# Kernel tuning notes

Hardware: AMD Instinct MI355X
Metric: run time of the kernel (lower is better)

## Reference

```python
import jax, jax.numpy as jnp
import numpy as np

DEPTH = 12
NODE_SIZE = 64
IN_SCALE = 1.0
SCALE = 0.1
IN_W = 1.8
SIZE = 2 ** DEPTH - 1          # 4095 total nodes
REST = SIZE - 1                # 4094 non-root nodes
M_BATCH = 128


def setup_inputs() -> dict:
    key = jax.random.key(0)
    k1, k2, k3 = jax.random.split(key, 3)
    weights = IN_W + 1e-4 * jax.random.normal(k1, (SIZE,), dtype=jnp.float32)
    noise_root = jax.random.normal(k2, (M_BATCH, NODE_SIZE, 1), dtype=jnp.float32)
    noise_rest = jax.random.normal(k3, (M_BATCH, NODE_SIZE, REST), dtype=jnp.float32)
    return {"weights": weights, "noise_root": noise_root, "noise_rest": noise_rest, "M": M_BATCH}


def reference(weights, noise_root, noise_rest, M):
    # Root: Normal(0, in_scale).rsample((M, node_size, 1))
    root = IN_SCALE * noise_root                      # (M, node, 1)
    samples_levels = [root]
    m_levels = []
    scale_levels = []
    off = 0
    for d in range(1, DEPTH):
        n = 2 ** d
        w = jax.nn.sigmoid(weights[off:off + n])       # (n,)
        parent = jnp.arange(n) // 2                    # half-index parent lookup
        m = w[None, None, :] * samples_levels[-1][:, :, parent]   # (M, node, n)
        sc = jnp.broadcast_to(((1.0 - w) * SCALE)[None, None, :], m.shape)
        samp = m + sc * noise_rest[:, :, off:off + n]  # reparameterized rsample
        samples_levels.append(samp)
        m_levels.append(m)
        scale_levels.append(sc)
        off += n
    samples = jnp.concatenate(samples_levels[::-1], axis=2)  # (M, node, 4095)
    ms = jnp.concatenate(m_levels[::-1], axis=2)              # (M, node, 4094)
    scales = jnp.concatenate(scale_levels[::-1], axis=2)      # (M, node, 4094)
    return samples, ms, scales
```

## Files before the change

kernel.cpp:

```cpp
#include <hip/hip_runtime.h>


constexpr int   kRows  = 8192;
constexpr float kScale = 0.1f;

typedef float f4_ __attribute__((ext_vector_type(4)));
typedef float f2_ __attribute__((ext_vector_type(2)));
typedef f4_ f4u __attribute__((aligned(4)));
typedef f2_ f2u __attribute__((aligned(4)));

__device__ __align__(16) float2 g_tab[4096];

__global__ __launch_bounds__(256) void lgt_precompute(
    const float* __restrict__ weights)
{
    int t = blockIdx.x * 256 + threadIdx.x;
    if (t < 4094) {
        int d = 31 - __clz(t + 2);
        int c = t + 4098 - 3 * (1 << d);
        float w = 1.0f / (1.0f + __expf(-weights[t]));
        g_tab[c] = make_float2(w, (1.0f - w) * kScale);
    }
}

__device__ __forceinline__ void lgkm_barrier() {
    __builtin_amdgcn_sched_barrier(0);
    asm volatile("s_waitcnt lgkmcnt(0)" ::: "memory");
    __builtin_amdgcn_s_barrier();
    __builtin_amdgcn_sched_barrier(0);
}

__global__ __launch_bounds__(256) void lgt_main(
    const float* __restrict__ noise_root,
    const float* __restrict__ noise_rest,
    float* __restrict__ samples,
    float* __restrict__ ms,
    float* __restrict__ scales)
{
    __shared__ float sL[256];

    const int row = blockIdx.x;
    const int tid = threadIdx.x;
    const float* __restrict__ nr = noise_rest + (size_t)row * 4094;
    float* __restrict__ sr = samples + (size_t)row * 4095;
    float* __restrict__ mr = ms      + (size_t)row * 4094;
    float* __restrict__ cr = scales  + (size_t)row * 4094;

    const float nzs = nr[tid];
    const float n8  = nr[254 + tid];
    const f2_  n9   = *(const f2_*)(nr + 510 + 2 * tid);
    const f2_  nA0  = *(const f2_*)(nr + 1022 + 4 * tid);
    const f2_  nA1  = *(const f2_*)(nr + 1022 + 4 * tid + 2);
    f2_ nL[4];
    #pragma unroll
    for (int k = 0; k < 4; ++k)
        nL[k] = *(const f2_*)(nr + 2046 + 8 * tid + 2 * k);
    const float rootv = noise_root[row];

    if (tid == 0) { sL[254] = rootv; sr[4094] = rootv; }
    lgkm_barrier();

    #pragma unroll
    for (int d = 1; d <= 7; ++d) {
        const int off     = (1 << d) - 2;
        const int n       = 1 << d;
        const int colbase = 4096 - (n << 1);
        if (tid >= off && tid < off + n) {
            const int c = colbase + (tid - off);
            const float2 t2 = g_tab[c];
            const float  p  = sL[(c >> 1) - 1792];
            const float  mv = t2.x * p;
            const float  v  = fmaf(t2.y, nzs, mv);
            sL[c - 3840] = v;
            sr[c] = v; mr[c] = mv; cr[c] = t2.y;
        }
        lgkm_barrier();
    }

    const float a7 = sL[tid >> 1];

    const float2 t8 = g_tab[3584 + tid];
    const float  m8 = t8.x * a7;
    const float  v8 = fmaf(t8.y, n8, m8);
    sr[3584 + tid] = v8; mr[3584 + tid] = m8; cr[3584 + tid] = t8.y;

    const f4_ t9 = *(const f4_*)(&g_tab[3072 + 2 * tid]);
    const float m90 = t9.x * v8, m91 = t9.z * v8;
    const float v90 = fmaf(t9.y, n9.x, m90);
    const float v91 = fmaf(t9.w, n9.y, m91);
    {
        f2_ sv; sv.x = v90; sv.y = v91;
        f2_ mv; mv.x = m90; mv.y = m91;
        f2_ cv; cv.x = t9.y; cv.y = t9.w;
        *(f2u*)(sr + 3072 + 2 * tid) = sv;
        *(f2_*)(mr + 3072 + 2 * tid) = mv;
        *(f2_*)(cr + 3072 + 2 * tid) = cv;
    }

    const f4_ tA = *(const f4_*)(&g_tab[2048 + 4 * tid]);
    const f4_ tB = *(const f4_*)(&g_tab[2048 + 4 * tid + 2]);
    const float mA0 = tA.x * v90, mA1 = tA.z * v90;
    const float mB0 = tB.x * v91, mB1 = tB.z * v91;
    const float vA0 = fmaf(tA.y, nA0.x, mA0);
    const float vA1 = fmaf(tA.w, nA0.y, mA1);
    const float vB0 = fmaf(tB.y, nA1.x, mB0);
    const float vB1 = fmaf(tB.w, nA1.y, mB1);
    {
        f4_ sv; sv.x = vA0; sv.y = vA1; sv.z = vB0; sv.w = vB1;
        f4_ mv; mv.x = mA0; mv.y = mA1; mv.z = mB0; mv.w = mB1;
        f4_ cv; cv.x = tA.y; cv.y = tA.w; cv.z = tB.y; cv.w = tB.w;
        *(f4u*)(sr + 2048 + 4 * tid) = sv;
        *(f4u*)(mr + 2048 + 4 * tid) = mv;
        *(f4u*)(cr + 2048 + 4 * tid) = cv;
    }

    const float pv0 = vA0, pv1 = vA1, pv2 = vB0, pv3 = vB1;
    float sv[8], mv[8], cv[8];
    #pragma unroll
    for (int k = 0; k < 4; ++k) {
        const f4_  t = *(const f4_*)(&g_tab[8 * tid + 2 * k]);
        const float p = (k == 0) ? pv0 : (k == 1) ? pv1 : (k == 2) ? pv2 : pv3;
        const float m0 = t.x * p, m1 = t.z * p;
        sv[2 * k]     = fmaf(t.y, nL[k].x, m0);
        sv[2 * k + 1] = fmaf(t.w, nL[k].y, m1);
        mv[2 * k] = m0; mv[2 * k + 1] = m1;
        cv[2 * k] = t.y; cv[2 * k + 1] = t.w;
    }
    {
        f4_ a, b;
        a.x = sv[0]; a.y = sv[1]; a.z = sv[2]; a.w = sv[3];
        b.x = sv[4]; b.y = sv[5]; b.z = sv[6]; b.w = sv[7];
        *(f4u*)(sr + 8 * tid)     = a;
        *(f4u*)(sr + 8 * tid + 4) = b;
        a.x = mv[0]; a.y = mv[1]; a.z = mv[2]; a.w = mv[3];
        b.x = mv[4]; b.y = mv[5]; b.z = mv[6]; b.w = mv[7];
        *(f4u*)(mr + 8 * tid)     = a;
        *(f4u*)(mr + 8 * tid + 4) = b;
        a.x = cv[0]; a.y = cv[1]; a.z = cv[2]; a.w = cv[3];
        b.x = cv[4]; b.y = cv[5]; b.z = cv[6]; b.w = cv[7];
        *(f4u*)(cr + 8 * tid)     = a;
        *(f4u*)(cr + 8 * tid + 4) = b;
    }
}

extern "C" void kernel_launch(void* const* d_in, const int* in_sizes, int n_in,
                              void* d_out, int out_size, void* d_ws, size_t ws_size,
                              hipStream_t stream)
{
    const float* weights    = (const float*)d_in[0];
    const float* noise_root = (const float*)d_in[1];
    const float* noise_rest = (const float*)d_in[2];

    float* out     = (float*)d_out;
    float* samples = out;
    float* ms      = samples + (size_t)kRows * 4095;
    float* scales  = ms      + (size_t)kRows * 4094;

    lgt_precompute<<<(4094 + 255) / 256, 256, 0, stream>>>(weights);
    lgt_main<<<kRows, 256, 0, stream>>>(noise_root, noise_rest,
                                        samples, ms, scales);
}
```

Before: 120.3 us.

## Split tree sampling into wave-per-row top kernel and barrier-free bulk kernel

Drops the sigmoid precompute table and computes sigmoid weights inline from the weights array. The shallow levels (1-7) are now done by a separate kernel, one wavefront per row, using shuffles instead of shared memory and block barriers. The bulk kernel then reads the level-7 values back from the samples output in global memory. This removes the serial barrier chain in each block of the main kernel. In exchange it adds a global round-trip for the level-7 values, a kernel launch, and extra transcendental work in every block.

Measured after the change: 130.5 us. +8.5%, slower.

```diff
diff --git a/kernel.cpp b/kernel.cpp
--- a/kernel.cpp
+++ b/kernel.cpp
@@ -9,137 +9,164 @@
 typedef f4_ f4u __attribute__((aligned(4)));
 typedef f2_ f2u __attribute__((aligned(4)));
 
-__device__ __align__(16) float2 g_tab[4096];
-
-__global__ __launch_bounds__(256) void lgt_precompute(
-    const float* __restrict__ weights)
-{
-    int t = blockIdx.x * 256 + threadIdx.x;
-    if (t < 4094) {
-        int d = 31 - __clz(t + 2);
-        int c = t + 4098 - 3 * (1 << d);
-        float w = 1.0f / (1.0f + __expf(-weights[t]));
-        g_tab[c] = make_float2(w, (1.0f - w) * kScale);
-    }
+__device__ __forceinline__ float sigm(float x) {
+    return 1.0f / (1.0f + __expf(-x));
 }
 
-__device__ __forceinline__ void lgkm_barrier() {
-    __builtin_amdgcn_sched_barrier(0);
-    asm volatile("s_waitcnt lgkmcnt(0)" ::: "memory");
-    __builtin_amdgcn_s_barrier();
-    __builtin_amdgcn_sched_barrier(0);
-}
-
-__global__ __launch_bounds__(256) void lgt_main(
+__global__ __launch_bounds__(256) void lgt_top(
+    const float* __restrict__ weights,
     const float* __restrict__ noise_root,
     const float* __restrict__ noise_rest,
     float* __restrict__ samples,
     float* __restrict__ ms,
     float* __restrict__ scales)
 {
-    __shared__ float sL[256];
-
-    const int row = blockIdx.x;
-    const int tid = threadIdx.x;
+    const int lane = threadIdx.x & 63;
+    const int row  = (blockIdx.x << 2) + (threadIdx.x >> 6);
     const float* __restrict__ nr = noise_rest + (size_t)row * 4094;
     float* __restrict__ sr = samples + (size_t)row * 4095;
     float* __restrict__ mr = ms      + (size_t)row * 4094;
     float* __restrict__ cr = scales  + (size_t)row * 4094;
 
-    const float nzs = nr[tid];
-    const float n8  = nr[254 + tid];
-    const f2_  n9   = *(const f2_*)(nr + 510 + 2 * tid);
-    const f2_  nA0  = *(const f2_*)(nr + 1022 + 4 * tid);
-    const f2_  nA1  = *(const f2_*)(nr + 1022 + 4 * tid + 2);
-    f2_ nL[4];
+    const float rootv = noise_root[row];
+    if (lane == 0) sr[4094] = rootv;
+
+    float v = rootv;
     #pragma unroll
-    for (int k = 0; k < 4; ++k)
-        nL[k] = *(const f2_*)(nr + 2046 + 8 * tid + 2 * k);
-    const float rootv = noise_root[row];
-
-    if (tid == 0) { sL[254] = rootv; sr[4094] = rootv; }
-    lgkm_barrier();
-
-    #pragma unroll
-    for (int d = 1; d <= 7; ++d) {
+    for (int d = 1; d <= 6; ++d) {
         const int off     = (1 << d) - 2;
         const int n       = 1 << d;
         const int colbase = 4096 - (n << 1);
-        if (tid >= off && tid < off + n) {
-            const int c = colbase + (tid - off);
-            const float2 t2 = g_tab[c];
-            const float  p  = sL[(c >> 1) - 1792];
-            const float  mv = t2.x * p;
-            const float  v  = fmaf(t2.y, nzs, mv);
-            sL[c - 3840] = v;
-            sr[c] = v; mr[c] = mv; cr[c] = t2.y;
+        const float p  = (d == 1) ? rootv : __shfl(v, lane >> 1);
+        const float wt = weights[off + lane];
+        const float nz = nr[off + lane];
+        const float w  = sigm(wt);
+        const float sc = (1.0f - w) * kScale;
+        const float m  = w * p;
+        v = fmaf(sc, nz, m);
+        if (lane < n) {
+            const int c = colbase + lane;
+            sr[c] = v; mr[c] = m; cr[c] = sc;
         }
-        lgkm_barrier();
     }
 
-    const float a7 = sL[tid >> 1];
+    {
+        const f2_ wt = *(const f2_*)(weights + 126 + 2 * lane);
+        const f2_ nz = *(const f2_*)(nr + 126 + 2 * lane);
+        const float w0  = sigm(wt.x), w1 = sigm(wt.y);
+        const float sc0 = (1.0f - w0) * kScale, sc1 = (1.0f - w1) * kScale;
+        const float m0  = w0 * v, m1 = w1 * v;
+        const float v0  = fmaf(sc0, nz.x, m0), v1 = fmaf(sc1, nz.y, m1);
+        const int   c   = 3840 + 2 * lane;
+        f2_ sv; sv.x = v0;  sv.y = v1;
+        f2_ mv; mv.x = m0;  mv.y = m1;
+        f2_ cv; cv.x = sc0; cv.y = sc1;
+        *(f2u*)(sr + c) = sv;
+        *(f2_*)(mr + c) = mv;
+        *(f2_*)(cr + c) = cv;
+    }
+}
 
-    const float2 t8 = g_tab[3584 + tid];
-    const float  m8 = t8.x * a7;
-    const float  v8 = fmaf(t8.y, n8, m8);
-    sr[3584 + tid] = v8; mr[3584 + tid] = m8; cr[3584 + tid] = t8.y;
+__global__ __launch_bounds__(256) void lgt_bulk(
+    const float* __restrict__ weights,
+    const float* __restrict__ noise_rest,
+    float*  samples,
+    float* __restrict__ ms,
+    float* __restrict__ scales)
+{
+    const int row = blockIdx.x;
+    const int s   = threadIdx.x;
+    const float* __restrict__ nr = noise_rest + (size_t)row * 4094;
+    float* sr = samples + (size_t)row * 4095;
+    float* __restrict__ mr = ms     + (size_t)row * 4094;
+    float* __restrict__ cr = scales + (size_t)row * 4094;
 
-    const f4_ t9 = *(const f4_*)(&g_tab[3072 + 2 * tid]);
-    const float m90 = t9.x * v8, m91 = t9.z * v8;
-    const float v90 = fmaf(t9.y, n9.x, m90);
-    const float v91 = fmaf(t9.w, n9.y, m91);
+    const float a7 = sr[3840 + (s >> 1)];
+
+    const float w8t = weights[254 + s];
+    const f2_  w9t  = *(const f2_*)(weights + 510  + 2 * s);
+    const f2_  wA0  = *(const f2_*)(weights + 1022 + 4 * s);
+    const f2_  wA1  = *(const f2_*)(weights + 1022 + 4 * s + 2);
+    f2_ wB[4];
+    #pragma unroll
+    for (int k = 0; k < 4; ++k)
+        wB[k] = *(const f2_*)(weights + 2046 + 8 * s + 2 * k);
+
+    const float n8 = nr[254 + s];
+    const f2_  n9  = *(const f2_*)(nr + 510  + 2 * s);
+    const f2_  nA0 = *(const f2_*)(nr + 1022 + 4 * s);
+    const f2_  nA1 = *(const f2_*)(nr + 1022 + 4 * s + 2);
+    f2_ nB[4];
+    #pragma unroll
+    for (int k = 0; k < 4; ++k)
+        nB[k] = *(const f2_*)(nr + 2046 + 8 * s + 2 * k);
+
+    const float w8  = sigm(w8t);
+    const float c8  = (1.0f - w8) * kScale;
+    const float m8  = w8 * a7;
+    const float v8  = fmaf(c8, n8, m8);
+    sr[3584 + s] = v8; mr[3584 + s] = m8; cr[3584 + s] = c8;
+
+    const float w90 = sigm(w9t.x), w91 = sigm(w9t.y);
+    const float c90 = (1.0f - w90) * kScale, c91 = (1.0f - w91) * kScale;
+    const float m90 = w90 * v8, m91 = w91 * v8;
+    const float v90 = fmaf(c90, n9.x, m90);
+    const float v91 = fmaf(c91, n9.y, m91);
     {
         f2_ sv; sv.x = v90; sv.y = v91;
         f2_ mv; mv.x = m90; mv.y = m91;
-        f2_ cv; cv.x = t9.y; cv.y = t9.w;
-        *(f2u*)(sr + 3072 + 2 * tid) = sv;
-        *(f2_*)(mr + 3072 + 2 * tid) = mv;
-        *(f2_*)(cr + 3072 + 2 * tid) = cv;
+        f2_ cv; cv.x = c90; cv.y = c91;
+        *(f2u*)(sr + 3072 + 2 * s) = sv;
+        *(f2_*)(mr + 3072 + 2 * s) = mv;
+        *(f2_*)(cr + 3072 + 2 * s) = cv;
     }
 
-    const f4_ tA = *(const f4_*)(&g_tab[2048 + 4 * tid]);
-    const f4_ tB = *(const f4_*)(&g_tab[2048 + 4 * tid + 2]);
-    const float mA0 = tA.x * v90, mA1 = tA.z * v90;
-    const float mB0 = tB.x * v91, mB1 = tB.z * v91;
-    const float vA0 = fmaf(tA.y, nA0.x, mA0);
-    const float vA1 = fmaf(tA.w, nA0.y, mA1);
-    const float vB0 = fmaf(tB.y, nA1.x, mB0);
-    const float vB1 = fmaf(tB.w, nA1.y, mB1);
+    const float wa0 = sigm(wA0.x), wa1 = sigm(wA0.y);
+    const float wa2 = sigm(wA1.x), wa3 = sigm(wA1.y);
+    const float ca0 = (1.0f - wa0) * kScale, ca1 = (1.0f - wa1) * kScale;
+    const float ca2 = (1.0f - wa2) * kScale, ca3 = (1.0f - wa3) * kScale;
+    const float mA0 = wa0 * v90, mA1 = wa1 * v90;
+    const float mA2 = wa2 * v91, mA3 = wa3 * v91;
+    const float vA0 = fmaf(ca0, nA0.x, mA0);
+    const float vA1 = fmaf(ca1, nA0.y, mA1);
+    const float vA2 = fmaf(ca2, nA1.x, mA2);
+    const float vA3 = fmaf(ca3, nA1.y, mA3);
     {
-        f4_ sv; sv.x = vA0; sv.y = vA1; sv.z = vB0; sv.w = vB1;
-        f4_ mv; mv.x = mA0; mv.y = mA1; mv.z = mB0; mv.w = mB1;
-        f4_ cv; cv.x = tA.y; cv.y = tA.w; cv.z = tB.y; cv.w = tB.w;
-        *(f4u*)(sr + 2048 + 4 * tid) = sv;
-        *(f4u*)(mr + 2048 + 4 * tid) = mv;
-        *(f4u*)(cr + 2048 + 4 * tid) = cv;
+        f4_ sv; sv.x = vA0; sv.y = vA1; sv.z = vA2; sv.w = vA3;
+        f4_ mv; mv.x = mA0; mv.y = mA1; mv.z = mA2; mv.w = mA3;
+        f4_ cv; cv.x = ca0; cv.y = ca1; cv.z = ca2; cv.w = ca3;
+        *(f4u*)(sr + 2048 + 4 * s) = sv;
+        *(f4u*)(mr + 2048 + 4 * s) = mv;
+        *(f4u*)(cr + 2048 + 4 * s) = cv;
     }
 
-    const float pv0 = vA0, pv1 = vA1, pv2 = vB0, pv3 = vB1;
+    const float pv[4] = { vA0, vA1, vA2, vA3 };
     float sv[8], mv[8], cv[8];
     #pragma unroll
     for (int k = 0; k < 4; ++k) {
-        const f4_  t = *(const f4_*)(&g_tab[8 * tid + 2 * k]);
-        const float p = (k == 0) ? pv0 : (k == 1) ? pv1 : (k == 2) ? pv2 : pv3;
-        const float m0 = t.x * p, m1 = t.z * p;
-        sv[2 * k]     = fmaf(t.y, nL[k].x, m0);
-        sv[2 * k + 1] = fmaf(t.w, nL[k].y, m1);
-        mv[2 * k] = m0; mv[2 * k + 1] = m1;
-        cv[2 * k] = t.y; cv[2 * k + 1] = t.w;
+        const float wb0 = sigm(wB[k].x), wb1 = sigm(wB[k].y);
+        const float cb0 = (1.0f - wb0) * kScale, cb1 = (1.0f - wb1) * kScale;
+        const float p   = pv[k];
+        const float mb0 = wb0 * p, mb1 = wb1 * p;
+        sv[2 * k]     = fmaf(cb0, nB[k].x, mb0);
+        sv[2 * k + 1] = fmaf(cb1, nB[k].y, mb1);
+        mv[2 * k] = mb0; mv[2 * k + 1] = mb1;
+        cv[2 * k] = cb0; cv[2 * k + 1] = cb1;
     }
     {
         f4_ a, b;
         a.x = sv[0]; a.y = sv[1]; a.z = sv[2]; a.w = sv[3];
         b.x = sv[4]; b.y = sv[5]; b.z = sv[6]; b.w = sv[7];
-        *(f4u*)(sr + 8 * tid)     = a;
-        *(f4u*)(sr + 8 * tid + 4) = b;
+        *(f4u*)(sr + 8 * s)     = a;
+        *(f4u*)(sr + 8 * s + 4) = b;
         a.x = mv[0]; a.y = mv[1]; a.z = mv[2]; a.w = mv[3];
         b.x = mv[4]; b.y = mv[5]; b.z = mv[6]; b.w = mv[7];
-        *(f4u*)(mr + 8 * tid)     = a;
-        *(f4u*)(mr + 8 * tid + 4) = b;
+        *(f4u*)(mr + 8 * s)     = a;
+        *(f4u*)(mr + 8 * s + 4) = b;
         a.x = cv[0]; a.y = cv[1]; a.z = cv[2]; a.w = cv[3];
         b.x = cv[4]; b.y = cv[5]; b.z = cv[6]; b.w = cv[7];
-        *(f4u*)(cr + 8 * tid)     = a;
-        *(f4u*)(cr + 8 * tid + 4) = b;
+        *(f4u*)(cr + 8 * s)     = a;
+        *(f4u*)(cr + 8 * s + 4) = b;
     }
 }
 
@@ -156,7 +183,8 @@
     float* ms      = samples + (size_t)kRows * 4095;
     float* scales  = ms      + (size_t)kRows * 4094;
 
-    lgt_precompute<<<(4094 + 255) / 256, 256, 0, stream>>>(weights);
-    lgt_main<<<kRows, 256, 0, stream>>>(noise_root, noise_rest,
+    lgt_top<<<kRows / 4, 256, 0, stream>>>(weights, noise_root, noise_rest,
+                                           samples, ms, scales);
+    lgt_bulk<<<kRows, 256, 0, stream>>>(weights, noise_rest,
                                         samples, ms, scales);
 }
```

## Split fused kernel into samples pass and separate ms/scales pass

Applied to the files above, without the earlier changes.

The single kernel that wrote samples, ms and scales is split in two. The first computes and writes only samples. The second reads the parent samples back from global memory and recomputes ms and scales with wide vector stores. This shrinks the register and store pressure of the dependency-chained first kernel, at the cost of an extra launch and roughly 128 MB of extra reads of samples.

Result: slower. 268.6 us (+123.2%).

```diff
diff --git a/kernel.cpp b/kernel.cpp
--- a/kernel.cpp
+++ b/kernel.cpp
@@ -30,12 +30,10 @@
     __builtin_amdgcn_sched_barrier(0);
 }
 
-__global__ __launch_bounds__(256) void lgt_main(
+__global__ __launch_bounds__(256) void lgt_samp(
     const float* __restrict__ noise_root,
     const float* __restrict__ noise_rest,
-    float* __restrict__ samples,
-    float* __restrict__ ms,
-    float* __restrict__ scales)
+    float* __restrict__ samples)
 {
     __shared__ float sL[256];
 
@@ -43,8 +41,6 @@
     const int tid = threadIdx.x;
     const float* __restrict__ nr = noise_rest + (size_t)row * 4094;
     float* __restrict__ sr = samples + (size_t)row * 4095;
-    float* __restrict__ mr = ms      + (size_t)row * 4094;
-    float* __restrict__ cr = scales  + (size_t)row * 4094;
 
     const float nzs = nr[tid];
     const float n8  = nr[254 + tid];
@@ -69,10 +65,9 @@
             const int c = colbase + (tid - off);
             const float2 t2 = g_tab[c];
             const float  p  = sL[(c >> 1) - 1792];
-            const float  mv = t2.x * p;
-            const float  v  = fmaf(t2.y, nzs, mv);
+            const float  v  = fmaf(t2.y, nzs, t2.x * p);
             sL[c - 3840] = v;
-            sr[c] = v; mr[c] = mv; cr[c] = t2.y;
+            sr[c] = v;
         }
         lgkm_barrier();
     }
@@ -80,51 +75,36 @@
     const float a7 = sL[tid >> 1];
 
     const float2 t8 = g_tab[3584 + tid];
-    const float  m8 = t8.x * a7;
-    const float  v8 = fmaf(t8.y, n8, m8);
-    sr[3584 + tid] = v8; mr[3584 + tid] = m8; cr[3584 + tid] = t8.y;
+    const float  v8 = fmaf(t8.y, n8, t8.x * a7);
+    sr[3584 + tid] = v8;
 
     const f4_ t9 = *(const f4_*)(&g_tab[3072 + 2 * tid]);
-    const float m90 = t9.x * v8, m91 = t9.z * v8;
-    const float v90 = fmaf(t9.y, n9.x, m90);
-    const float v91 = fmaf(t9.w, n9.y, m91);
+    const float v90 = fmaf(t9.y, n9.x, t9.x * v8);
+    const float v91 = fmaf(t9.w, n9.y, t9.z * v8);
     {
         f2_ sv; sv.x = v90; sv.y = v91;
-        f2_ mv; mv.x = m90; mv.y = m91;
-        f2_ cv; cv.x = t9.y; cv.y = t9.w;
         *(f2u*)(sr + 3072 + 2 * tid) = sv;
-        *(f2_*)(mr + 3072 + 2 * tid) = mv;
-        *(f2_*)(cr + 3072 + 2 * tid) = cv;
     }
 
     const f4_ tA = *(const f4_*)(&g_tab[2048 + 4 * tid]);
     const f4_ tB = *(const f4_*)(&g_tab[2048 + 4 * tid + 2]);
-    const float mA0 = tA.x * v90, mA1 = tA.z * v90;
-    const float mB0 = tB.x * v91, mB1 = tB.z * v91;
-    const float vA0 = fmaf(tA.y, nA0.x, mA0);
-    const float vA1 = fmaf(tA.w, nA0.y, mA1);
-    const float vB0 = fmaf(tB.y, nA1.x, mB0);
-    const float vB1 = fmaf(tB.w, nA1.y, mB1);
+    const float vA0 = fmaf(tA.y, nA0.x, tA.x * v90);
+    const float vA1 = fmaf(tA.w, nA0.y, tA.z * v90);
+    const float vA2 = fmaf(tB.y, nA1.x, tB.x * v91);
+    const float vA3 = fmaf(tB.w, nA1.y, tB.z * v91);
     {
-        f4_ sv; sv.x = vA0; sv.y = vA1; sv.z = vB0; sv.w = vB1;
-        f4_ mv; mv.x = mA0; mv.y = mA1; mv.z = mB0; mv.w = mB1;
-        f4_ cv; cv.x = tA.y; cv.y = tA.w; cv.z = tB.y; cv.w = tB.w;
+        f4_ sv; sv.x = vA0; sv.y = vA1; sv.z = vA2; sv.w = vA3;
         *(f4u*)(sr + 2048 + 4 * tid) = sv;
-        *(f4u*)(mr + 2048 + 4 * tid) = mv;
-        *(f4u*)(cr + 2048 + 4 * tid) = cv;
     }
 
-    const float pv0 = vA0, pv1 = vA1, pv2 = vB0, pv3 = vB1;
-    float sv[8], mv[8], cv[8];
+    const float pv[4] = { vA0, vA1, vA2, vA3 };
+    float sv[8];
     #pragma unroll
     for (int k = 0; k < 4; ++k) {
         const f4_  t = *(const f4_*)(&g_tab[8 * tid + 2 * k]);
-        const float p = (k == 0) ? pv0 : (k == 1) ? pv1 : (k == 2) ? pv2 : pv3;
-        const float m0 = t.x * p, m1 = t.z * p;
-        sv[2 * k]     = fmaf(t.y, nL[k].x, m0);
-        sv[2 * k + 1] = fmaf(t.w, nL[k].y, m1);
-        mv[2 * k] = m0; mv[2 * k + 1] = m1;
-        cv[2 * k] = t.y; cv[2 * k + 1] = t.w;
+        const float p = pv[k];
+        sv[2 * k]     = fmaf(t.y, nL[k].x, t.x * p);
+        sv[2 * k + 1] = fmaf(t.w, nL[k].y, t.z * p);
     }
     {
         f4_ a, b;
@@ -132,14 +112,44 @@
         b.x = sv[4]; b.y = sv[5]; b.z = sv[6]; b.w = sv[7];
         *(f4u*)(sr + 8 * tid)     = a;
         *(f4u*)(sr + 8 * tid + 4) = b;
-        a.x = mv[0]; a.y = mv[1]; a.z = mv[2]; a.w = mv[3];
-        b.x = mv[4]; b.y = mv[5]; b.z = mv[6]; b.w = mv[7];
-        *(f4u*)(mr + 8 * tid)     = a;
-        *(f4u*)(mr + 8 * tid + 4) = b;
-        a.x = cv[0]; a.y = cv[1]; a.z = cv[2]; a.w = cv[3];
-        b.x = cv[4]; b.y = cv[5]; b.z = cv[6]; b.w = cv[7];
-        *(f4u*)(cr + 8 * tid)     = a;
-        *(f4u*)(cr + 8 * tid + 4) = b;
+    }
+}
+
+__global__ __launch_bounds__(256) void lgt_msc(
+    const float* __restrict__ samples,
+    float* __restrict__ ms,
+    float* __restrict__ scales)
+{
+    const int row = blockIdx.x;
+    const int t   = threadIdx.x;
+    const float* __restrict__ sp = samples + (size_t)row * 4095;
+    float* __restrict__ mr = ms     + (size_t)row * 4094;
+    float* __restrict__ cr = scales + (size_t)row * 4094;
+
+    #pragma unroll
+    for (int i = 0; i < 4; ++i) {
+        const int c = (t << 4) + (i << 2);
+        if (c + 3 < 4094) {
+            const f4_ ta = *(const f4_*)(&g_tab[c]);
+            const f4_ tb = *(const f4_*)(&g_tab[c + 2]);
+            const f2u pp = *(const f2u*)(sp + (c >> 1) + 2048);
+            f4_ mv, cv;
+            mv.x = ta.x * pp.x; mv.y = ta.z * pp.x;
+            mv.z = tb.x * pp.y; mv.w = tb.z * pp.y;
+            cv.x = ta.y; cv.y = ta.w; cv.z = tb.y; cv.w = tb.w;
+            *(f4u*)(mr + c) = mv;
+            *(f4u*)(cr + c) = cv;
+        } else {
+            #pragma unroll
+            for (int e = 0; e < 4; ++e) {
+                const int ce = c + e;
+                if (ce < 4094) {
+                    const float2 tt = g_tab[ce];
+                    mr[ce] = tt.x * sp[(ce >> 1) + 2048];
+                    cr[ce] = tt.y;
+                }
+            }
+        }
     }
 }
 
@@ -157,6 +167,6 @@
     float* scales  = ms      + (size_t)kRows * 4094;
 
     lgt_precompute<<<(4094 + 255) / 256, 256, 0, stream>>>(weights);
-    lgt_main<<<kRows, 256, 0, stream>>>(noise_root, noise_rest,
-                                        samples, ms, scales);
+    lgt_samp<<<kRows, 256, 0, stream>>>(noise_root, noise_rest, samples);
+    lgt_msc<<<kRows, 256, 0, stream>>>(samples, ms, scales);
 }
```

## Replace shared-memory level barriers with redundant per-wave shuffle tree

Applied to the files above, without the earlier changes.

Drops the shared-memory buffer and the seven block-wide barriers used for the top tree levels. Each wavefront now computes levels 1-7 redundantly in registers, passing parents with cross-lane shuffles, and only wave 0 writes those outputs. Level 7 values are then shuffled to form the level-8 parent inside each wave. This removes barrier stalls and LDS round trips at the cost of duplicated ALU work, extra noise and table loads per wave, and extra shuffle instructions.

After: 141.4 us. 1.18x slower.

```diff
diff --git a/kernel.cpp b/kernel.cpp
--- a/kernel.cpp
+++ b/kernel.cpp
@@ -23,13 +23,6 @@
     }
 }
 
-__device__ __forceinline__ void lgkm_barrier() {
-    __builtin_amdgcn_sched_barrier(0);
-    asm volatile("s_waitcnt lgkmcnt(0)" ::: "memory");
-    __builtin_amdgcn_s_barrier();
-    __builtin_amdgcn_sched_barrier(0);
-}
-
 __global__ __launch_bounds__(256) void lgt_main(
     const float* __restrict__ noise_root,
     const float* __restrict__ noise_rest,
@@ -37,16 +30,16 @@
     float* __restrict__ ms,
     float* __restrict__ scales)
 {
-    __shared__ float sL[256];
+    const int row  = blockIdx.x;
+    const int tid  = threadIdx.x;
+    const int lane = tid & 63;
+    const int wv   = tid >> 6;
 
-    const int row = blockIdx.x;
-    const int tid = threadIdx.x;
     const float* __restrict__ nr = noise_rest + (size_t)row * 4094;
     float* __restrict__ sr = samples + (size_t)row * 4095;
     float* __restrict__ mr = ms      + (size_t)row * 4094;
     float* __restrict__ cr = scales  + (size_t)row * 4094;
 
-    const float nzs = nr[tid];
     const float n8  = nr[254 + tid];
     const f2_  n9   = *(const f2_*)(nr + 510 + 2 * tid);
     const f2_  nA0  = *(const f2_*)(nr + 1022 + 4 * tid);
@@ -55,29 +48,47 @@
     #pragma unroll
     for (int k = 0; k < 4; ++k)
         nL[k] = *(const f2_*)(nr + 2046 + 8 * tid + 2 * k);
+
     const float rootv = noise_root[row];
+    if (tid == 0) sr[4094] = rootv;
 
-    if (tid == 0) { sL[254] = rootv; sr[4094] = rootv; }
-    lgkm_barrier();
-
+    float v = rootv;
     #pragma unroll
-    for (int d = 1; d <= 7; ++d) {
+    for (int d = 1; d <= 6; ++d) {
         const int off     = (1 << d) - 2;
         const int n       = 1 << d;
         const int colbase = 4096 - (n << 1);
-        if (tid >= off && tid < off + n) {
-            const int c = colbase + (tid - off);
-            const float2 t2 = g_tab[c];
-            const float  p  = sL[(c >> 1) - 1792];
-            const float  mv = t2.x * p;
-            const float  v  = fmaf(t2.y, nzs, mv);
-            sL[c - 3840] = v;
-            sr[c] = v; mr[c] = mv; cr[c] = t2.y;
+        const int i       = lane & (n - 1);
+        const float p  = (d == 1) ? rootv : __shfl(v, lane >> 1);
+        const float2 t2 = g_tab[colbase + i];
+        const float  nz = nr[off + i];
+        const float  m  = t2.x * p;
+        v = fmaf(t2.y, nz, m);
+        if (wv == 0 && lane < n) {
+            const int c = colbase + lane;
+            sr[c] = v; mr[c] = m; cr[c] = t2.y;
         }
-        lgkm_barrier();
     }
 
-    const float a7 = sL[tid >> 1];
+    const f4_ t7 = *(const f4_*)(&g_tab[3840 + 2 * lane]);
+    const f2_ n7 = *(const f2_*)(nr + 126 + 2 * lane);
+    const float m70 = t7.x * v,  m71 = t7.z * v;
+    const float v70 = fmaf(t7.y, n7.x, m70);
+    const float v71 = fmaf(t7.w, n7.y, m71);
+    if (wv == 0) {
+        const int c = 3840 + 2 * lane;
+        f2_ sv; sv.x = v70; sv.y = v71;
+        f2_ mv; mv.x = m70; mv.y = m71;
+        f2_ cv; cv.x = t7.y; cv.y = t7.w;
+        *(f2u*)(sr + c) = sv;
+        *(f2_*)(mr + c) = mv;
+        *(f2_*)(cr + c) = cv;
+    }
+
+    const int   src = (wv << 4) + (lane >> 2);
+    const float a70 = __shfl(v70, src);
+    const float a71 = __shfl(v71, src);
+    const float a7  = ((lane >> 1) & 1) ? a71 : a70;
 
     const float2 t8 = g_tab[3584 + tid];
     const float  m8 = t8.x * a7;
@@ -100,26 +111,26 @@
     const f4_ tA = *(const f4_*)(&g_tab[2048 + 4 * tid]);
     const f4_ tB = *(const f4_*)(&g_tab[2048 + 4 * tid + 2]);
     const float mA0 = tA.x * v90, mA1 = tA.z * v90;
-    const float mB0 = tB.x * v91, mB1 = tB.z * v91;
+    const float mA2 = tB.x * v91, mA3 = tB.z * v91;
     const float vA0 = fmaf(tA.y, nA0.x, mA0);
     const float vA1 = fmaf(tA.w, nA0.y, mA1);
-    const float vB0 = fmaf(tB.y, nA1.x, mB0);
-    const float vB1 = fmaf(tB.w, nA1.y, mB1);
+    const float vA2 = fmaf(tB.y, nA1.x, mA2);
+    const float vA3 = fmaf(tB.w, nA1.y, mA3);
     {
-        f4_ sv; sv.x = vA0; sv.y = vA1; sv.z = vB0; sv.w = vB1;
-        f4_ mv; mv.x = mA0; mv.y = mA1; mv.z = mB0; mv.w = mB1;
+        f4_ sv; sv.x = vA0; sv.y = vA1; sv.z = vA2; sv.w = vA3;
+        f4_ mv; mv.x = mA0; mv.y = mA1; mv.z = mA2; mv.w = mA3;
         f4_ cv; cv.x = tA.y; cv.y = tA.w; cv.z = tB.y; cv.w = tB.w;
         *(f4u*)(sr + 2048 + 4 * tid) = sv;
         *(f4u*)(mr + 2048 + 4 * tid) = mv;
         *(f4u*)(cr + 2048 + 4 * tid) = cv;
     }
 
-    const float pv0 = vA0, pv1 = vA1, pv2 = vB0, pv3 = vB1;
+    const float pv[4] = { vA0, vA1, vA2, vA3 };
     float sv[8], mv[8], cv[8];
     #pragma unroll
     for (int k = 0; k < 4; ++k) {
         const f4_  t = *(const f4_*)(&g_tab[8 * tid + 2 * k]);
-        const float p = (k == 0) ? pv0 : (k == 1) ? pv1 : (k == 2) ? pv2 : pv3;
+        const float p = pv[k];
         const float m0 = t.x * p, m1 = t.z * p;
         sv[2 * k]     = fmaf(t.y, nL[k].x, m0);
         sv[2 * k + 1] = fmaf(t.w, nL[k].y, m1);
```
